# Optimization experiments

Measured on AMD Instinct MI355X. Metric: run time of the kernel, lower is better.

## Reference

```python
import jax, jax.numpy as jnp
import numpy as np

B = 2048       # batch
POOL = 512     # e_prompt_pool_size
TOPK = 4       # top_k
EPL = 8        # e_prompt_length
GPL = 8        # g_prompt_length
EMB = 768      # emb_d
KEYD = 768     # key_dim


def setup_inputs() -> dict:
    key = jax.random.key(0)
    k1, k2, k3, k4, k5 = jax.random.split(key, 5)
    return {
        "x_querry": jax.random.normal(k1, (B, KEYD), dtype=jnp.float32),
        "x_block": jax.random.normal(k2, (B, EMB), dtype=jnp.float32),
        "e_k": jax.random.uniform(k3, (POOL, KEYD), dtype=jnp.float32),
        "e_p": jax.random.uniform(k4, (POOL, EPL, EMB), dtype=jnp.float32),
        "g_p": jax.random.uniform(k5, (GPL, EMB), dtype=jnp.float32),
        "l": 0,
    }


def _l2norm(x, eps=1e-12):
    # matches torch F.normalize(dim=-1): x / max(||x||, eps)
    n = jnp.sqrt(jnp.sum(x * x, axis=-1, keepdims=True))
    return x / jnp.maximum(n, eps)


def reference(x_querry, x_block, e_k, e_p, g_p, l):
    # ---- E-prompt routing (l in e_layers) ----
    n_K = _l2norm(e_k)                              # [P, C]
    q = jax.lax.stop_gradient(_l2norm(x_querry))    # [B, C], detached in torch
    cos_sim = jnp.einsum('bj,kj->bk', q, n_K)       # [B, P]
    distance = 1.0 - cos_sim
    # use_contrastiv=False -> mass = 1.0
    scaled_distance = distance * 1.0
    # torch.topk(largest=False) == top_k of negated values
    _, k_idx = jax.lax.top_k(-scaled_distance, TOPK)   # [B, K]
    P_ = e_p[k_idx]                                  # [B, K, EPL, EMB] gather
    # non-contrastive loss: (1 - cos_sim[:, k_idx]).mean() -> [B, B, K] mean
    loss = jnp.mean(1.0 - cos_sim[:, k_idx])
    i = EPL // 2
    Ek = P_[:, :, :i, :].reshape(B, -1, EMB)         # [B, K*i, EMB]
    Ev = P_[:, :, i:, :].reshape(B, -1, EMB)
    # count scatter (train_count update)
    counts = jnp.bincount(k_idx.reshape(-1), length=POOL)

    # ---- G-prompt (l in g_layers) ----
    j = GPL // 2
    Gk = jnp.broadcast_to(g_p[:j], (B, j, EMB))
    Gv = jnp.broadcast_to(g_p[j:], (B, GPL - j, EMB))

    Pk = jnp.concatenate([Ek, Gk], axis=1)           # [B, K*i + j, EMB]
    Pv = jnp.concatenate([Ev, Gv], axis=1)
    return Pk, Pv, loss, counts, x_block
```

## Files before the change

### kernel.cpp

```cpp
#include <hip/hip_runtime.h>
#include <hip/hip_bf16.h>
#include <math.h>

static constexpr int NB    = 2048;
static constexpr int NPOOL = 512;
static constexpr int NTOPK = 4;
static constexpr int NEPL  = 8;
static constexpr int NEMB  = 768;
static constexpr int NSLOT = 20;
static constexpr int NCAND = 8;

__global__ __launch_bounds__(256) void norms_kernel(
    const float* __restrict__ xq, const float* __restrict__ ek,
    double* __restrict__ qn, double* __restrict__ kn,
    float* __restrict__ rqn, float* __restrict__ rkn) {
  int row = blockIdx.x;
  const float* src;
  double* dst;
  float* rdst;
  if (row < NB) { src = xq + (size_t)row * NEMB; dst = qn + row; rdst = rqn + row; }
  else          { src = ek + (size_t)(row - NB) * NEMB; dst = kn + (row - NB); rdst = rkn + (row - NB); }
  double s = 0.0;
  for (int i = threadIdx.x; i < NEMB; i += 256) {
    double v = (double)src[i];
    s += v * v;
  }
  for (int off = 32; off > 0; off >>= 1) s += __shfl_down(s, off, 64);
  __shared__ double red[4];
  if ((threadIdx.x & 63) == 0) red[threadIdx.x >> 6] = s;
  __syncthreads();
  if (threadIdx.x == 0) {
    double n = sqrt(red[0] + red[1] + red[2] + red[3]);
    *dst = n;
    *rdst = (float)(1.0 / fmax(n, 1e-12));
  }
}

__global__ __launch_bounds__(256) void cos_kernel(
    const float* __restrict__ xq, const float* __restrict__ ek,
    const float* __restrict__ rqn, const float* __restrict__ rkn,
    float* __restrict__ cosm) {
  __shared__ float As[32][68];
  __shared__ float Bs[32][68];
  const int t = threadIdx.x;
  const int tx = t & 15;
  const int ty = t >> 4;
  const int bp = blockIdx.x * 64;
  const int bb = blockIdx.y * 64;
  float acc[4][4] = {};
  for (int k0 = 0; k0 < NEMB; k0 += 32) {
#pragma unroll
    for (int uu = 0; uu < 2; uu++) {
      int u = t + uu * 256;
      int m = u >> 3;
      int k4 = (u & 7) * 4;
      float4 a = *(const float4*)(xq + (size_t)(bb + m) * NEMB + k0 + k4);
      float4 b = *(const float4*)(ek + (size_t)(bp + m) * NEMB + k0 + k4);
      As[k4 + 0][m] = a.x; As[k4 + 1][m] = a.y; As[k4 + 2][m] = a.z; As[k4 + 3][m] = a.w;
      Bs[k4 + 0][m] = b.x; Bs[k4 + 1][m] = b.y; Bs[k4 + 2][m] = b.z; Bs[k4 + 3][m] = b.w;
    }
    __syncthreads();
#pragma unroll
    for (int kk = 0; kk < 32; kk++) {
      float4 av = *(const float4*)&As[kk][ty * 4];
      float4 bv = *(const float4*)&Bs[kk][tx * 4];
      acc[0][0] = fmaf(av.x, bv.x, acc[0][0]); acc[0][1] = fmaf(av.x, bv.y, acc[0][1]);
      acc[0][2] = fmaf(av.x, bv.z, acc[0][2]); acc[0][3] = fmaf(av.x, bv.w, acc[0][3]);
      acc[1][0] = fmaf(av.y, bv.x, acc[1][0]); acc[1][1] = fmaf(av.y, bv.y, acc[1][1]);
      acc[1][2] = fmaf(av.y, bv.z, acc[1][2]); acc[1][3] = fmaf(av.y, bv.w, acc[1][3]);
      acc[2][0] = fmaf(av.z, bv.x, acc[2][0]); acc[2][1] = fmaf(av.z, bv.y, acc[2][1]);
      acc[2][2] = fmaf(av.z, bv.z, acc[2][2]); acc[2][3] = fmaf(av.z, bv.w, acc[2][3]);
      acc[3][0] = fmaf(av.w, bv.x, acc[3][0]); acc[3][1] = fmaf(av.w, bv.y, acc[3][1]);
      acc[3][2] = fmaf(av.w, bv.z, acc[3][2]); acc[3][3] = fmaf(av.w, bv.w, acc[3][3]);
    }
    __syncthreads();
  }
  float4 rk = *(const float4*)&rkn[bp + tx * 4];
#pragma unroll
  for (int i = 0; i < 4; i++) {
    float rq = rqn[bb + ty * 4 + i];
    float4 cv;
    cv.x = acc[i][0] * rq * rk.x;
    cv.y = acc[i][1] * rq * rk.y;
    cv.z = acc[i][2] * rq * rk.z;
    cv.w = acc[i][3] * rq * rk.w;
    *(float4*)(cosm + (size_t)(bb + ty * 4 + i) * NPOOL + bp + tx * 4) = cv;
  }
}

__device__ __forceinline__ bool btf(float av, int ai, float bv, int bi) {
  return (av > bv) || (av == bv && ai < bi);
}
__device__ __forceinline__ bool btd(double av, int ai, double bv, int bi) {
  return (av > bv) || (av == bv && ai < bi);
}
#define CE(a, b)                                                        \
  do {                                                                  \
    if (!btf(v[a], vi[a], v[b], vi[b])) {                               \
      float tv = v[a]; v[a] = v[b]; v[b] = tv;                          \
      int ti = vi[a]; vi[a] = vi[b]; vi[b] = ti;                        \
    }                                                                   \
  } while (0)

__global__ __launch_bounds__(256) void topk_kernel(
    const float* __restrict__ cosm, const float* __restrict__ xq,
    const float* __restrict__ ek, const double* __restrict__ qn,
    const double* __restrict__ kn, int* __restrict__ kidx,
    int* __restrict__ counts) {
  int wave = threadIdx.x >> 6, lane = threadIdx.x & 63;
  int row = blockIdx.x * 4 + wave;
  const float* crow = cosm + (size_t)row * NPOOL;
  float v[8]; int vi[8];
#pragma unroll
  for (int j = 0; j < 8; j++) {
    int p = j * 64 + lane;
    v[j] = crow[p];
    vi[j] = p;
  }
  CE(0,1); CE(2,3); CE(4,5); CE(6,7);
  CE(0,2); CE(1,3); CE(4,6); CE(5,7);
  CE(1,2); CE(5,6);
  CE(0,4); CE(1,5); CE(2,6); CE(3,7);
  CE(2,4); CE(3,5);
  CE(1,2); CE(3,4); CE(5,6);
#pragma unroll
  for (int off = 1; off < 64; off <<= 1) {
    float ov[8]; int oi[8];
#pragma unroll
    for (int m = 0; m < 8; m++) {
      ov[m] = __shfl_xor(v[m], off, 64);
      oi[m] = __shfl_xor(vi[m], off, 64);
    }
#pragma unroll
    for (int m = 0; m < 8; m++) {
      if (!btf(v[m], vi[m], ov[7 - m], oi[7 - m])) { v[m] = ov[7 - m]; vi[m] = oi[7 - m]; }
    }
    CE(0,4); CE(1,5); CE(2,6); CE(3,7);
    CE(0,2); CE(1,3); CE(4,6); CE(5,7);
    CE(0,1); CE(2,3); CE(4,5); CE(6,7);
  }
  const float* xrow = xq + (size_t)row * NEMB;
  double xr[12];
#pragma unroll
  for (int e = 0; e < 12; e++) xr[e] = (double)xrow[lane * 12 + e];
  double qmax = fmax(qn[row], 1e-12);
  double cand[8];
#pragma unroll
  for (int c = 0; c < 8; c++) {
    int pi = vi[c];
    const float* kb = ek + (size_t)pi * NEMB + lane * 12;
    double s = 0.0;
#pragma unroll
    for (int e = 0; e < 12; e++) s = fma(xr[e], (double)kb[e], s);
#pragma unroll
    for (int off = 1; off < 64; off <<= 1) s += __shfl_xor(s, off, 64);
    cand[c] = s / (qmax * fmax(kn[pi], 1e-12));
  }
  bool used[8] = {false, false, false, false, false, false, false, false};
#pragma unroll
  for (int m = 0; m < NTOPK; m++) {
    int best = -1;
#pragma unroll
    for (int c = 0; c < 8; c++) {
      if (!used[c] && (best < 0 || btd(cand[c], vi[c], cand[best], vi[best]))) best = c;
    }
    used[best] = true;
    if (lane == 0) {
      kidx[row * 4 + m] = vi[best];
      atomicAdd(&counts[vi[best]], 1);
    }
  }
}
#undef CE

__global__ __launch_bounds__(256) void colsum_kernel(
    const float* __restrict__ cosm, double* __restrict__ S) {
  int p = blockIdx.x * 256 + threadIdx.x;
  int r0 = blockIdx.y * 128;
  double s = 0.0;
  for (int r = r0; r < r0 + 128; r++) s += (double)cosm[(size_t)r * NPOOL + p];
  atomicAdd(&S[p], s);
}

__global__ __launch_bounds__(256) void loss_counts_kernel(
    const double* __restrict__ S, const int* __restrict__ counts,
    float* __restrict__ out_loss, float* __restrict__ out_counts) {
  double s = 0.0;
  for (int p = threadIdx.x; p < NPOOL; p += 256) {
    int c = counts[p];
    out_counts[p] = (float)c;
    s += (double)c * S[p];
  }
  for (int off = 32; off > 0; off >>= 1) s += __shfl_down(s, off, 64);
  __shared__ double red[4];
  if ((threadIdx.x & 63) == 0) red[threadIdx.x >> 6] = s;
  __syncthreads();
  if (threadIdx.x == 0) {
    double total = red[0] + red[1] + red[2] + red[3];
    *out_loss = (float)(1.0 - total / (double)((long long)NB * NB * NTOPK));
  }
}

__global__ __launch_bounds__(256) void gather_kernel(
    const float* __restrict__ e_p, const float* __restrict__ g_p,
    const int* __restrict__ kidx, const float* __restrict__ x_block,
    float* __restrict__ Pk, float* __restrict__ Pv,
    float* __restrict__ out_xb) {
  int b = blockIdx.x;
  __shared__ int idx[4];
  if (threadIdx.x < 4) idx[threadIdx.x] = kidx[b * 4 + threadIdx.x];
  __syncthreads();
  float4* dk = (float4*)(Pk + (size_t)b * NSLOT * NEMB);
  float4* dv = (float4*)(Pv + (size_t)b * NSLOT * NEMB);
  const int R = NEMB / 4;
  for (int u = threadIdx.x; u < NSLOT * R; u += 256) {
    int s = u / R;
    int r = u - s * R;
    const float4* sk;
    const float4* sv;
    if (s < 16) {
      int pi = idx[s >> 2];
      int t = s & 3;
      const float* basek = e_p + ((size_t)pi * NEPL + t) * NEMB;
      sk = (const float4*)basek;
      sv = (const float4*)(basek + 4 * NEMB);
    } else {
      sk = (const float4*)(g_p + (size_t)(s - 16) * NEMB);
      sv = (const float4*)(g_p + (size_t)(s - 16 + 4) * NEMB);
    }
    dk[u] = sk[r];
    dv[u] = sv[r];
  }
  for (int i = threadIdx.x; i < NEMB; i += 256)
    out_xb[(size_t)b * NEMB + i] = x_block[(size_t)b * NEMB + i];
}

extern "C" void kernel_launch(void* const* d_in, const int* in_sizes, int n_in,
                              void* d_out, int out_size, void* d_ws, size_t ws_size,
                              hipStream_t stream) {
  const float* x_querry = (const float*)d_in[0];
  const float* x_block  = (const float*)d_in[1];
  const float* e_k      = (const float*)d_in[2];
  const float* e_p      = (const float*)d_in[3];
  const float* g_p      = (const float*)d_in[4];

  double* qn     = (double*)d_ws;
  double* kn     = qn + NB;
  double* S      = kn + NPOOL;
  float*  rqn    = (float*)(S + NPOOL);
  float*  rkn    = rqn + NB;
  float*  cosm   = rkn + NPOOL;
  int*    kidx   = (int*)(cosm + (size_t)NB * NPOOL);
  int*    counts = kidx + NB * NTOPK;

  float* out        = (float*)d_out;
  float* Pk         = out;
  float* Pv         = Pk + (size_t)NB * NSLOT * NEMB;
  float* out_loss   = Pv + (size_t)NB * NSLOT * NEMB;
  float* out_counts = out_loss + 1;
  float* out_xb     = out_counts + NPOOL;

  hipMemsetAsync(S, 0, NPOOL * sizeof(double), stream);
  hipMemsetAsync(counts, 0, NPOOL * sizeof(int), stream);

  norms_kernel<<<NB + NPOOL, 256, 0, stream>>>(x_querry, e_k, qn, kn, rqn, rkn);
  cos_kernel<<<dim3(NPOOL / 64, NB / 64), 256, 0, stream>>>(x_querry, e_k, rqn, rkn, cosm);
  topk_kernel<<<NB / 4, 256, 0, stream>>>(cosm, x_querry, e_k, qn, kn, kidx, counts);
  colsum_kernel<<<dim3(NPOOL / 256, NB / 128), 256, 0, stream>>>(cosm, S);
  loss_counts_kernel<<<1, 256, 0, stream>>>(S, counts, out_loss, out_counts);
  gather_kernel<<<NB, 256, 0, stream>>>(e_p, g_p, kidx, x_block, Pk, Pv, out_xb);
}
```

Baseline: 383.7 us.

## Fuse top-k with gather and compute loss via query-sum algebra

Top-k selection and the prompt gather now run in one kernel, one row per block, so the kidx round trip and a separate launch go away. The loss no longer needs a column sum over the cosine matrix. It is computed as the sum of normalized queries dotted with a count-weighted sum of normalized keys. That sum is built from an extra cos_kernel block column and a small 3-block loss kernel that uses a done-counter finish. The memsets move into an extra norms block, and one wave per block does the top-k while the other waves wait at the barrier.

Measured after the change: 426.4 us. +11.1%, slower.

```diff
diff --git a/kernel.cpp b/kernel.cpp
--- a/kernel.cpp
+++ b/kernel.cpp
@@ -1,5 +1,4 @@
 #include <hip/hip_runtime.h>
-#include <hip/hip_bf16.h>
 #include <math.h>
 
 static constexpr int NB    = 2048;
@@ -8,18 +7,25 @@
 static constexpr int NEPL  = 8;
 static constexpr int NEMB  = 768;
 static constexpr int NSLOT = 20;
-static constexpr int NCAND = 8;
 
 __global__ __launch_bounds__(256) void norms_kernel(
     const float* __restrict__ xq, const float* __restrict__ ek,
-    double* __restrict__ qn, double* __restrict__ kn,
-    float* __restrict__ rqn, float* __restrict__ rkn) {
+    double* __restrict__ qinv, double* __restrict__ kinv,
+    float* __restrict__ rqn, float* __restrict__ rkn,
+    double* __restrict__ u, double* __restrict__ lacc,
+    int* __restrict__ done, int* __restrict__ counts) {
   int row = blockIdx.x;
+  if (row == NB + NPOOL) {
+    for (int i = threadIdx.x; i < NEMB; i += 256) u[i] = 0.0;
+    for (int i = threadIdx.x; i < NPOOL; i += 256) counts[i] = 0;
+    if (threadIdx.x == 0) { *lacc = 0.0; *done = 0; }
+    return;
+  }
   const float* src;
-  double* dst;
+  double* dinv;
   float* rdst;
-  if (row < NB) { src = xq + (size_t)row * NEMB; dst = qn + row; rdst = rqn + row; }
-  else          { src = ek + (size_t)(row - NB) * NEMB; dst = kn + (row - NB); rdst = rkn + (row - NB); }
+  if (row < NB) { src = xq + (size_t)row * NEMB; dinv = qinv + row; rdst = rqn + row; }
+  else          { src = ek + (size_t)(row - NB) * NEMB; dinv = kinv + (row - NB); rdst = rkn + (row - NB); }
   double s = 0.0;
   for (int i = threadIdx.x; i < NEMB; i += 256) {
     double v = (double)src[i];
@@ -31,15 +37,34 @@
   __syncthreads();
   if (threadIdx.x == 0) {
     double n = sqrt(red[0] + red[1] + red[2] + red[3]);
-    *dst = n;
-    *rdst = (float)(1.0 / fmax(n, 1e-12));
+    double inv = 1.0 / fmax(n, 1e-12);
+    *dinv = inv;
+    *rdst = (float)inv;
   }
 }
 
 __global__ __launch_bounds__(256) void cos_kernel(
     const float* __restrict__ xq, const float* __restrict__ ek,
     const float* __restrict__ rqn, const float* __restrict__ rkn,
-    float* __restrict__ cosm) {
+    const double* __restrict__ qinv, float* __restrict__ cosm,
+    double* __restrict__ u) {
+  if (blockIdx.x >= NPOOL / 64) {
+    int b = (blockIdx.x - NPOOL / 64) * (NB / 64) + blockIdx.y;
+    int c0 = threadIdx.x;
+    int r0 = b * 32;
+    double s0 = 0.0, s1 = 0.0, s2 = 0.0;
+    for (int r = r0; r < r0 + 32; r++) {
+      double inv = qinv[r];
+      const float* xr = xq + (size_t)r * NEMB;
+      s0 = fma((double)xr[c0], inv, s0);
+      s1 = fma((double)xr[c0 + 256], inv, s1);
+      s2 = fma((double)xr[c0 + 512], inv, s2);
+    }
+    atomicAdd(&u[c0], s0);
+    atomicAdd(&u[c0 + 256], s1);
+    atomicAdd(&u[c0 + 512], s2);
+    return;
+  }
   __shared__ float As[32][68];
   __shared__ float Bs[32][68];
   const int t = threadIdx.x;
@@ -51,13 +76,13 @@
   for (int k0 = 0; k0 < NEMB; k0 += 32) {
 #pragma unroll
     for (int uu = 0; uu < 2; uu++) {
-      int u = t + uu * 256;
-      int m = u >> 3;
-      int k4 = (u & 7) * 4;
+      int uidx = t + uu * 256;
+      int m = uidx >> 3;
+      int k4 = (uidx & 7) * 4;
       float4 a = *(const float4*)(xq + (size_t)(bb + m) * NEMB + k0 + k4);
-      float4 b = *(const float4*)(ek + (size_t)(bp + m) * NEMB + k0 + k4);
+      float4 bvv = *(const float4*)(ek + (size_t)(bp + m) * NEMB + k0 + k4);
       As[k4 + 0][m] = a.x; As[k4 + 1][m] = a.y; As[k4 + 2][m] = a.z; As[k4 + 3][m] = a.w;
-      Bs[k4 + 0][m] = b.x; Bs[k4 + 1][m] = b.y; Bs[k4 + 2][m] = b.z; Bs[k4 + 3][m] = b.w;
+      Bs[k4 + 0][m] = bvv.x; Bs[k4 + 1][m] = bvv.y; Bs[k4 + 2][m] = bvv.z; Bs[k4 + 3][m] = bvv.w;
     }
     __syncthreads();
 #pragma unroll
@@ -102,137 +127,136 @@
     }                                                                   \
   } while (0)
 
-__global__ __launch_bounds__(256) void topk_kernel(
+__global__ __launch_bounds__(256) void topk_gather_kernel(
     const float* __restrict__ cosm, const float* __restrict__ xq,
-    const float* __restrict__ ek, const double* __restrict__ qn,
-    const double* __restrict__ kn, int* __restrict__ kidx,
-    int* __restrict__ counts) {
-  int wave = threadIdx.x >> 6, lane = threadIdx.x & 63;
-  int row = blockIdx.x * 4 + wave;
-  const float* crow = cosm + (size_t)row * NPOOL;
-  float v[8]; int vi[8];
-#pragma unroll
-  for (int j = 0; j < 8; j++) {
-    int p = j * 64 + lane;
-    v[j] = crow[p];
-    vi[j] = p;
-  }
-  CE(0,1); CE(2,3); CE(4,5); CE(6,7);
-  CE(0,2); CE(1,3); CE(4,6); CE(5,7);
-  CE(1,2); CE(5,6);
-  CE(0,4); CE(1,5); CE(2,6); CE(3,7);
-  CE(2,4); CE(3,5);
-  CE(1,2); CE(3,4); CE(5,6);
-#pragma unroll
-  for (int off = 1; off < 64; off <<= 1) {
-    float ov[8]; int oi[8];
-#pragma unroll
-    for (int m = 0; m < 8; m++) {
-      ov[m] = __shfl_xor(v[m], off, 64);
-      oi[m] = __shfl_xor(vi[m], off, 64);
-    }
-#pragma unroll
-    for (int m = 0; m < 8; m++) {
-      if (!btf(v[m], vi[m], ov[7 - m], oi[7 - m])) { v[m] = ov[7 - m]; vi[m] = oi[7 - m]; }
-    }
+    const float* __restrict__ ek, const double* __restrict__ qinv,
+    const double* __restrict__ kinv, const float* __restrict__ e_p,
+    const float* __restrict__ g_p, const float* __restrict__ x_block,
+    int* __restrict__ counts, float* __restrict__ Pk, float* __restrict__ Pv,
+    float* __restrict__ out_xb) {
+  const int row = blockIdx.x;
+  __shared__ int sidx[4];
+  const int wave = threadIdx.x >> 6, lane = threadIdx.x & 63;
+  if (wave == 0) {
+    const float* crow = cosm + (size_t)row * NPOOL;
+    float v[8]; int vi[8];
+#pragma unroll
+    for (int j = 0; j < 8; j++) {
+      int p = j * 64 + lane;
+      v[j] = crow[p];
+      vi[j] = p;
+    }
+    CE(0,1); CE(2,3); CE(4,5); CE(6,7);
+    CE(0,2); CE(1,3); CE(4,6); CE(5,7);
+    CE(1,2); CE(5,6);
     CE(0,4); CE(1,5); CE(2,6); CE(3,7);
-    CE(0,2); CE(1,3); CE(4,6); CE(5,7);
-    CE(0,1); CE(2,3); CE(4,5); CE(6,7);
-  }
-  const float* xrow = xq + (size_t)row * NEMB;
-  double xr[12];
-#pragma unroll
-  for (int e = 0; e < 12; e++) xr[e] = (double)xrow[lane * 12 + e];
-  double qmax = fmax(qn[row], 1e-12);
-  double cand[8];
-#pragma unroll
-  for (int c = 0; c < 8; c++) {
-    int pi = vi[c];
-    const float* kb = ek + (size_t)pi * NEMB + lane * 12;
-    double s = 0.0;
-#pragma unroll
-    for (int e = 0; e < 12; e++) s = fma(xr[e], (double)kb[e], s);
-#pragma unroll
-    for (int off = 1; off < 64; off <<= 1) s += __shfl_xor(s, off, 64);
-    cand[c] = s / (qmax * fmax(kn[pi], 1e-12));
-  }
-  bool used[8] = {false, false, false, false, false, false, false, false};
-#pragma unroll
-  for (int m = 0; m < NTOPK; m++) {
-    int best = -1;
+    CE(2,4); CE(3,5);
+    CE(1,2); CE(3,4); CE(5,6);
+#pragma unroll
+    for (int off = 1; off < 64; off <<= 1) {
+      float ov[8]; int oi[8];
+#pragma unroll
+      for (int m = 0; m < 8; m++) {
+        ov[m] = __shfl_xor(v[m], off, 64);
+        oi[m] = __shfl_xor(vi[m], off, 64);
+      }
+#pragma unroll
+      for (int m = 0; m < 8; m++) {
+        if (!btf(v[m], vi[m], ov[7 - m], oi[7 - m])) { v[m] = ov[7 - m]; vi[m] = oi[7 - m]; }
+      }
+      CE(0,4); CE(1,5); CE(2,6); CE(3,7);
+      CE(0,2); CE(1,3); CE(4,6); CE(5,7);
+      CE(0,1); CE(2,3); CE(4,5); CE(6,7);
+    }
+    const float* xrow = xq + (size_t)row * NEMB;
+    double xr[12];
+#pragma unroll
+    for (int e = 0; e < 12; e++) xr[e] = (double)xrow[lane * 12 + e];
+    double qi = qinv[row];
+    double cand[8];
 #pragma unroll
     for (int c = 0; c < 8; c++) {
-      if (!used[c] && (best < 0 || btd(cand[c], vi[c], cand[best], vi[best]))) best = c;
-    }
-    used[best] = true;
-    if (lane == 0) {
-      kidx[row * 4 + m] = vi[best];
-      atomicAdd(&counts[vi[best]], 1);
-    }
-  }
-}
-#undef CE
-
-__global__ __launch_bounds__(256) void colsum_kernel(
-    const float* __restrict__ cosm, double* __restrict__ S) {
-  int p = blockIdx.x * 256 + threadIdx.x;
-  int r0 = blockIdx.y * 128;
-  double s = 0.0;
-  for (int r = r0; r < r0 + 128; r++) s += (double)cosm[(size_t)r * NPOOL + p];
-  atomicAdd(&S[p], s);
-}
-
-__global__ __launch_bounds__(256) void loss_counts_kernel(
-    const double* __restrict__ S, const int* __restrict__ counts,
-    float* __restrict__ out_loss, float* __restrict__ out_counts) {
-  double s = 0.0;
-  for (int p = threadIdx.x; p < NPOOL; p += 256) {
-    int c = counts[p];
-    out_counts[p] = (float)c;
-    s += (double)c * S[p];
-  }
-  for (int off = 32; off > 0; off >>= 1) s += __shfl_down(s, off, 64);
-  __shared__ double red[4];
-  if ((threadIdx.x & 63) == 0) red[threadIdx.x >> 6] = s;
-  __syncthreads();
-  if (threadIdx.x == 0) {
-    double total = red[0] + red[1] + red[2] + red[3];
-    *out_loss = (float)(1.0 - total / (double)((long long)NB * NB * NTOPK));
-  }
-}
-
-__global__ __launch_bounds__(256) void gather_kernel(
-    const float* __restrict__ e_p, const float* __restrict__ g_p,
-    const int* __restrict__ kidx, const float* __restrict__ x_block,
-    float* __restrict__ Pk, float* __restrict__ Pv,
-    float* __restrict__ out_xb) {
-  int b = blockIdx.x;
-  __shared__ int idx[4];
-  if (threadIdx.x < 4) idx[threadIdx.x] = kidx[b * 4 + threadIdx.x];
-  __syncthreads();
-  float4* dk = (float4*)(Pk + (size_t)b * NSLOT * NEMB);
-  float4* dv = (float4*)(Pv + (size_t)b * NSLOT * NEMB);
+      int pi = vi[c];
+      const float* kb = ek + (size_t)pi * NEMB + lane * 12;
+      double s = 0.0;
+#pragma unroll
+      for (int e = 0; e < 12; e++) s = fma(xr[e], (double)kb[e], s);
+#pragma unroll
+      for (int off = 1; off < 64; off <<= 1) s += __shfl_xor(s, off, 64);
+      cand[c] = s * qi * kinv[pi];
+    }
+    bool used[8] = {false, false, false, false, false, false, false, false};
+#pragma unroll
+    for (int m = 0; m < NTOPK; m++) {
+      int best = -1;
+#pragma unroll
+      for (int c = 0; c < 8; c++) {
+        if (!used[c] && (best < 0 || btd(cand[c], vi[c], cand[best], vi[best]))) best = c;
+      }
+      used[best] = true;
+      if (lane == 0) {
+        sidx[m] = vi[best];
+        atomicAdd(&counts[vi[best]], 1);
+      }
+    }
+  }
+  __syncthreads();
+  float4* dk = (float4*)(Pk + (size_t)row * NSLOT * NEMB);
+  float4* dv = (float4*)(Pv + (size_t)row * NSLOT * NEMB);
   const int R = NEMB / 4;
-  for (int u = threadIdx.x; u < NSLOT * R; u += 256) {
-    int s = u / R;
-    int r = u - s * R;
+  for (int uidx = threadIdx.x; uidx < NSLOT * R; uidx += 256) {
+    int s = uidx / R;
+    int r = uidx - s * R;
     const float4* sk;
     const float4* sv;
     if (s < 16) {
-      int pi = idx[s >> 2];
-      int t = s & 3;
-      const float* basek = e_p + ((size_t)pi * NEPL + t) * NEMB;
+      int pi = sidx[s >> 2];
+      int tt = s & 3;
+      const float* basek = e_p + ((size_t)pi * NEPL + tt) * NEMB;
       sk = (const float4*)basek;
       sv = (const float4*)(basek + 4 * NEMB);
     } else {
       sk = (const float4*)(g_p + (size_t)(s - 16) * NEMB);
       sv = (const float4*)(g_p + (size_t)(s - 16 + 4) * NEMB);
     }
-    dk[u] = sk[r];
-    dv[u] = sv[r];
+    dk[uidx] = sk[r];
+    dv[uidx] = sv[r];
   }
   for (int i = threadIdx.x; i < NEMB; i += 256)
-    out_xb[(size_t)b * NEMB + i] = x_block[(size_t)b * NEMB + i];
+    out_xb[(size_t)row * NEMB + i] = x_block[(size_t)row * NEMB + i];
+}
+#undef CE
+
+__global__ __launch_bounds__(256) void loss_kernel(
+    const float* __restrict__ ek, const double* __restrict__ kinv,
+    const double* __restrict__ u, const int* __restrict__ counts,
+    double* __restrict__ lacc, int* __restrict__ done,
+    float* __restrict__ out_loss, float* __restrict__ out_counts) {
+  __shared__ double tp[NPOOL];
+  for (int p = threadIdx.x; p < NPOOL; p += 256) {
+    int c = counts[p];
+    tp[p] = (double)c * kinv[p];
+    if (blockIdx.x == 0) out_counts[p] = (float)c;
+  }
+  __syncthreads();
+  const int j = blockIdx.x * 256 + threadIdx.x;
+  double m = 0.0;
+  for (int p = 0; p < NPOOL; p++) m = fma(tp[p], (double)ek[(size_t)p * NEMB + j], m);
+  double part = m * u[j];
+  for (int off = 32; off > 0; off >>= 1) part += __shfl_down(part, off, 64);
+  __shared__ double red[4];
+  if ((threadIdx.x & 63) == 0) red[threadIdx.x >> 6] = part;
+  __syncthreads();
+  if (threadIdx.x == 0) {
+    double tot = red[0] + red[1] + red[2] + red[3];
+    atomicAdd(lacc, tot);
+    __threadfence();
+    int d = atomicAdd(done, 1);
+    if (d == 2) {
+      double total = atomicAdd(lacc, 0.0);
+      *out_loss = (float)(1.0 - total / (double)((long long)NB * NB * NTOPK));
+    }
+  }
 }
 
 extern "C" void kernel_launch(void* const* d_in, const int* in_sizes, int n_in,
@@ -244,14 +268,15 @@
   const float* e_p      = (const float*)d_in[3];
   const float* g_p      = (const float*)d_in[4];
 
-  double* qn     = (double*)d_ws;
-  double* kn     = qn + NB;
-  double* S      = kn + NPOOL;
-  float*  rqn    = (float*)(S + NPOOL);
+  double* qinv   = (double*)d_ws;
+  double* kinv   = qinv + NB;
+  double* u      = kinv + NPOOL;
+  double* lacc   = u + NEMB;
+  int*    done   = (int*)(lacc + 1);
+  float*  rqn    = (float*)(done + 2);
   float*  rkn    = rqn + NB;
   float*  cosm   = rkn + NPOOL;
-  int*    kidx   = (int*)(cosm + (size_t)NB * NPOOL);
-  int*    counts = kidx + NB * NTOPK;
+  int*    counts = (int*)(cosm + (size_t)NB * NPOOL);
 
   float* out        = (float*)d_out;
   float* Pk         = out;
@@ -260,13 +285,12 @@
   float* out_counts = out_loss + 1;
   float* out_xb     = out_counts + NPOOL;
 
-  hipMemsetAsync(S, 0, NPOOL * sizeof(double), stream);
-  hipMemsetAsync(counts, 0, NPOOL * sizeof(int), stream);
-
-  norms_kernel<<<NB + NPOOL, 256, 0, stream>>>(x_querry, e_k, qn, kn, rqn, rkn);
-  cos_kernel<<<dim3(NPOOL / 64, NB / 64), 256, 0, stream>>>(x_querry, e_k, rqn, rkn, cosm);
-  topk_kernel<<<NB / 4, 256, 0, stream>>>(cosm, x_querry, e_k, qn, kn, kidx, counts);
-  colsum_kernel<<<dim3(NPOOL / 256, NB / 128), 256, 0, stream>>>(cosm, S);
-  loss_counts_kernel<<<1, 256, 0, stream>>>(S, counts, out_loss, out_counts);
-  gather_kernel<<<NB, 256, 0, stream>>>(e_p, g_p, kidx, x_block, Pk, Pv, out_xb);
-}
+  norms_kernel<<<NB + NPOOL + 1, 256, 0, stream>>>(
+      x_querry, e_k, qinv, kinv, rqn, rkn, u, lacc, done, counts);
+  cos_kernel<<<dim3(NPOOL / 64 + 2, NB / 64), 256, 0, stream>>>(
+      x_querry, e_k, rqn, rkn, qinv, cosm, u);
+  topk_gather_kernel<<<NB, 256, 0, stream>>>(
+      cosm, x_querry, e_k, qinv, kinv, e_p, g_p, x_block, counts, Pk, Pv, out_xb);
+  loss_kernel<<<3, 256, 0, stream>>>(
+      e_k, kinv, u, counts, lacc, done, out_loss, out_counts);
+}
```

## Compute cosine similarity with split-bf16 MFMA instead of fp32 SIMT GEMM

Applied to the files above, without the earlier changes.

The norms kernel now also splits x_querry and e_k into bf16 high and low parts, and a new MFMA kernel computes the cosine matrix with three bf16 products (hh, hl, lh) so accuracy stays close to fp32. It runs only when the workspace is large enough, otherwise the old fp32 tiled kernel is used. The x_block copy is also changed to mostly float4 stores. The new path adds workspace traffic for the split operands and relies on the top-k stage's fp64 refinement to tolerate the small precision loss.

Result: no change. 378.7 us (-1.3%).

```diff
diff --git a/kernel.cpp b/kernel.cpp
--- a/kernel.cpp
+++ b/kernel.cpp
@@ -1,5 +1,4 @@
 #include <hip/hip_runtime.h>
-#include <hip/hip_bf16.h>
 #include <math.h>
 
 static constexpr int NB    = 2048;
@@ -8,22 +7,48 @@
 static constexpr int NEPL  = 8;
 static constexpr int NEMB  = 768;
 static constexpr int NSLOT = 20;
-static constexpr int NCAND = 8;
+
+typedef unsigned short u16;
+typedef __attribute__((ext_vector_type(8))) short bf16x8;
+typedef __attribute__((ext_vector_type(4))) float f32x4;
 
 __global__ __launch_bounds__(256) void norms_kernel(
     const float* __restrict__ xq, const float* __restrict__ ek,
     double* __restrict__ qn, double* __restrict__ kn,
-    float* __restrict__ rqn, float* __restrict__ rkn) {
+    float* __restrict__ rqn, float* __restrict__ rkn,
+    u16* __restrict__ xqh, u16* __restrict__ xql,
+    u16* __restrict__ ekh, u16* __restrict__ ekl) {
   int row = blockIdx.x;
   const float* src;
   double* dst;
   float* rdst;
-  if (row < NB) { src = xq + (size_t)row * NEMB; dst = qn + row; rdst = rqn + row; }
-  else          { src = ek + (size_t)(row - NB) * NEMB; dst = kn + (row - NB); rdst = rkn + (row - NB); }
+  u16* hh;
+  u16* ll;
+  if (row < NB) {
+    src = xq + (size_t)row * NEMB; dst = qn + row; rdst = rqn + row;
+    hh = xqh ? xqh + (size_t)row * NEMB : nullptr;
+    ll = xql ? xql + (size_t)row * NEMB : nullptr;
+  } else {
+    int r = row - NB;
+    src = ek + (size_t)r * NEMB; dst = kn + r; rdst = rkn + r;
+    hh = ekh ? ekh + (size_t)r * NEMB : nullptr;
+    ll = ekl ? ekl + (size_t)r * NEMB : nullptr;
+  }
   double s = 0.0;
   for (int i = threadIdx.x; i < NEMB; i += 256) {
-    double v = (double)src[i];
-    s += v * v;
+    float a = src[i];
+    s += (double)a * (double)a;
+    if (hh) {
+      unsigned u = __float_as_uint(a);
+      unsigned r = u + 0x7fff + ((u >> 16) & 1);
+      u16 h = (u16)(r >> 16);
+      float hf = __uint_as_float((unsigned)h << 16);
+      float res = a - hf;
+      unsigned ul = __float_as_uint(res);
+      unsigned rl = ul + 0x7fff + ((ul >> 16) & 1);
+      hh[i] = h;
+      ll[i] = (u16)(rl >> 16);
+    }
   }
   for (int off = 32; off > 0; off >>= 1) s += __shfl_down(s, off, 64);
   __shared__ double red[4];
@@ -33,6 +58,68 @@
     double n = sqrt(red[0] + red[1] + red[2] + red[3]);
     *dst = n;
     *rdst = (float)(1.0 / fmax(n, 1e-12));
+  }
+}
+
+__global__ __launch_bounds__(512) void cos_mfma_kernel(
+    const u16* __restrict__ xqh, const u16* __restrict__ xql,
+    const u16* __restrict__ ekh, const u16* __restrict__ ekl,
+    const float* __restrict__ rqn, const float* __restrict__ rkn,
+    float* __restrict__ cosm) {
+  const int t = threadIdx.x;
+  const int lane = t & 63, w = t >> 6;
+  const int mw = (w & 3) * 16;
+  const int nh = (w >> 2) * 32;
+  const int bp = blockIdx.x * 64, bb = blockIdx.y * 64;
+  const int lr = lane & 15, kg = (lane >> 4) * 8;
+  const size_t arow  = (size_t)(bb + mw + lr) * NEMB + kg;
+  const size_t brow0 = (size_t)(bp + nh + lr) * NEMB + kg;
+  const size_t brow1 = (size_t)(bp + nh + 16 + lr) * NEMB + kg;
+  const u16* pah  = xqh + arow;
+  const u16* pal  = xql + arow;
+  const u16* pb0h = ekh + brow0;
+  const u16* pb0l = ekl + brow0;
+  const u16* pb1h = ekh + brow1;
+  const u16* pb1l = ekl + brow1;
+  f32x4 acc0 = {0.f, 0.f, 0.f, 0.f};
+  f32x4 acc1 = {0.f, 0.f, 0.f, 0.f};
+
+  bf16x8 ah  = *(const bf16x8*)(pah);
+  bf16x8 al  = *(const bf16x8*)(pal);
+  bf16x8 b0h = *(const bf16x8*)(pb0h);
+  bf16x8 b0l = *(const bf16x8*)(pb0l);
+  bf16x8 b1h = *(const bf16x8*)(pb1h);
+  bf16x8 b1l = *(const bf16x8*)(pb1l);
+#pragma unroll
+  for (int ks = 1; ks <= NEMB / 32; ks++) {
+    bf16x8 nah, nal, nb0h, nb0l, nb1h, nb1l;
+    if (ks < NEMB / 32) {
+      const int o = ks * 32;
+      nah  = *(const bf16x8*)(pah + o);
+      nal  = *(const bf16x8*)(pal + o);
+      nb0h = *(const bf16x8*)(pb0h + o);
+      nb0l = *(const bf16x8*)(pb0l + o);
+      nb1h = *(const bf16x8*)(pb1h + o);
+      nb1l = *(const bf16x8*)(pb1l + o);
+    }
+    acc0 = __builtin_amdgcn_mfma_f32_16x16x32_bf16(ah, b0h, acc0, 0, 0, 0);
+    acc1 = __builtin_amdgcn_mfma_f32_16x16x32_bf16(ah, b1h, acc1, 0, 0, 0);
+    acc0 = __builtin_amdgcn_mfma_f32_16x16x32_bf16(ah, b0l, acc0, 0, 0, 0);
+    acc1 = __builtin_amdgcn_mfma_f32_16x16x32_bf16(ah, b1l, acc1, 0, 0, 0);
+    acc0 = __builtin_amdgcn_mfma_f32_16x16x32_bf16(al, b0h, acc0, 0, 0, 0);
+    acc1 = __builtin_amdgcn_mfma_f32_16x16x32_bf16(al, b1h, acc1, 0, 0, 0);
+    if (ks < NEMB / 32) {
+      ah = nah; al = nal; b0h = nb0h; b0l = nb0l; b1h = nb1h; b1l = nb1l;
+    }
+  }
+  const float rk0 = rkn[bp + nh + lr];
+  const float rk1 = rkn[bp + nh + 16 + lr];
+  const int r0 = bb + mw + (lane >> 4) * 4;
+#pragma unroll
+  for (int j = 0; j < 4; j++) {
+    const float rq = rqn[r0 + j];
+    cosm[(size_t)(r0 + j) * NPOOL + bp + nh + lr]      = acc0[j] * rq * rk0;
+    cosm[(size_t)(r0 + j) * NPOOL + bp + nh + 16 + lr] = acc1[j] * rq * rk1;
   }
 }
 
@@ -231,8 +318,15 @@
     dk[u] = sk[r];
     dv[u] = sv[r];
   }
-  for (int i = threadIdx.x; i < NEMB; i += 256)
-    out_xb[(size_t)b * NEMB + i] = x_block[(size_t)b * NEMB + i];
+  const float* xsrc = x_block + (size_t)b * NEMB;
+  float* xdst = out_xb + (size_t)b * NEMB;
+  if (threadIdx.x < 3) xdst[threadIdx.x] = xsrc[threadIdx.x];
+  if (threadIdx.x == 3) xdst[NEMB - 1] = xsrc[NEMB - 1];
+  for (int k = threadIdx.x; k < 191; k += 256) {
+    int i = 3 + 4 * k;
+    float4 vv = make_float4(xsrc[i], xsrc[i + 1], xsrc[i + 2], xsrc[i + 3]);
+    *(float4*)(xdst + i) = vv;
+  }
 }
 
 extern "C" void kernel_launch(void* const* d_in, const int* in_sizes, int n_in,
@@ -252,6 +346,13 @@
   float*  cosm   = rkn + NPOOL;
   int*    kidx   = (int*)(cosm + (size_t)NB * NPOOL);
   int*    counts = kidx + NB * NTOPK;
+  u16*    xqh    = (u16*)(counts + NPOOL);
+  u16*    xql    = xqh + (size_t)NB * NEMB;
+  u16*    ekh    = xql + (size_t)NB * NEMB;
+  u16*    ekl    = ekh + (size_t)NPOOL * NEMB;
+  const size_t ws_need =
+      (size_t)((char*)(ekl + (size_t)NPOOL * NEMB) - (char*)d_ws);
+  const bool use_mfma = ws_size >= ws_need;
 
   float* out        = (float*)d_out;
   float* Pk         = out;
@@ -263,8 +364,17 @@
   hipMemsetAsync(S, 0, NPOOL * sizeof(double), stream);
   hipMemsetAsync(counts, 0, NPOOL * sizeof(int), stream);
 
-  norms_kernel<<<NB + NPOOL, 256, 0, stream>>>(x_querry, e_k, qn, kn, rqn, rkn);
-  cos_kernel<<<dim3(NPOOL / 64, NB / 64), 256, 0, stream>>>(x_querry, e_k, rqn, rkn, cosm);
+  norms_kernel<<<NB + NPOOL, 256, 0, stream>>>(
+      x_querry, e_k, qn, kn, rqn, rkn,
+      use_mfma ? xqh : nullptr, use_mfma ? xql : nullptr,
+      use_mfma ? ekh : nullptr, use_mfma ? ekl : nullptr);
+  if (use_mfma) {
+    cos_mfma_kernel<<<dim3(NPOOL / 64, NB / 64), 512, 0, stream>>>(
+        xqh, xql, ekh, ekl, rqn, rkn, cosm);
+  } else {
+    cos_kernel<<<dim3(NPOOL / 64, NB / 64), 256, 0, stream>>>(
+        x_querry, e_k, rqn, rkn, cosm);
+  }
   topk_kernel<<<NB / 4, 256, 0, stream>>>(cosm, x_querry, e_k, qn, kn, kidx, counts);
   colsum_kernel<<<dim3(NPOOL / 256, NB / 128), 256, 0, stream>>>(cosm, S);
   loss_counts_kernel<<<1, 256, 0, stream>>>(S, counts, out_loss, out_counts);
```
